# Kernel tuning notes

Measured on AMD Instinct MI355X. Metric: run time of the kernel, lower is better.

The kernel has to match this reference:

```python
import jax, jax.numpy as jnp
import numpy as np

NUM_HEADS = 16
HEAD_DIM = 64
TAU = 0.07
EPS = 1e-12  # torch F.normalize eps


def setup_inputs() -> dict:
    key = jax.random.key(0)
    ks = jax.random.split(key, 12)
    B, L, D = 4, 2048, 1024
    s = 1.0 / np.sqrt(D)
    inp = {
        'q': jax.random.normal(ks[0], (B, L, D), jnp.float32),
        'k': jax.random.normal(ks[1], (B, L, D), jnp.float32),
        'v': jax.random.normal(ks[2], (B, L, D), jnp.float32),
        'Wq': jax.random.normal(ks[3], (D, D), jnp.float32) * s,
        'bq': jax.random.normal(ks[4], (D,), jnp.float32) * 0.01,
        'Wk': jax.random.normal(ks[5], (D, D), jnp.float32) * s,
        'bk': jax.random.normal(ks[6], (D,), jnp.float32) * 0.01,
        'Wv': jax.random.normal(ks[7], (D, D), jnp.float32) * s,
        'bv': jax.random.normal(ks[8], (D,), jnp.float32) * 0.01,
        'Wo': jax.random.normal(ks[9], (D, D), jnp.float32) * s,
        'bo': jax.random.normal(ks[10], (D,), jnp.float32) * 0.01,
    }
    return inp


def _split(x):
    b, l, d = x.shape
    return x.reshape(b, l, NUM_HEADS, HEAD_DIM).transpose(0, 2, 1, 3)  # [b,h,l,dh]


def _l2norm(x):
    n = jnp.sqrt(jnp.sum(x * x, axis=-1, keepdims=True))
    return x / jnp.maximum(n, EPS)


def reference(q, k, v, Wq, bq, Wk, bk, Wv, bv, Wo, bo):
    # Linear projections (torch Linear: y = x @ W.T + b)
    qh = _l2norm(_split(q @ Wq.T + bq))
    kh = _l2norm(_split(k @ Wk.T + bk))
    vh = _split(v @ Wv.T + bv)
    scores = jnp.einsum('bhqd,bhkd->bhqk', qh, kh) / max(TAU, 1e-6)
    attn = jax.nn.softmax(scores, axis=-1)  # dropout = identity in eval
    out = jnp.einsum('bhqk,bhkd->bhqd', attn, vh)
    b, h, l, dh = out.shape
    merged = out.transpose(0, 2, 1, 3).reshape(b, l, h * dh)
    return merged @ Wo.T + bo
```

## Files before the change

kernel.cpp:

```cpp
#include <hip/hip_runtime.h>

#define BB 4
#define LL 2048
#define DD 1024
#define NH 16
#define DH 64
#define MM (BB*LL)

typedef _Float16 half8 __attribute__((ext_vector_type(8)));
typedef _Float16 half4 __attribute__((ext_vector_type(4)));
typedef _Float16 half2 __attribute__((ext_vector_type(2)));
typedef float floatx4 __attribute__((ext_vector_type(4)));

__device__ __forceinline__ void gload_lds16(const void* g, void* l) {
    __builtin_amdgcn_global_load_lds((const __attribute__((address_space(1))) void*)g,
                                     (__attribute__((address_space(3))) void*)l,
                                     16, 0, 0);
}

__device__ __forceinline__ floatx4 mfma16(half8 a, half8 b, floatx4 c) {
    return __builtin_amdgcn_mfma_f32_16x16x32_f16(a, b, c, 0, 0, 0);
}

__global__ __launch_bounds__(256) void cvt_f32_f16(const float* __restrict__ s,
                                                   _Float16* __restrict__ d, int n4) {
    int i = blockIdx.x * 256 + threadIdx.x;
    if (i < n4) {
        float4 f = ((const float4*)s)[i];
        half4 h;
        h[0] = (_Float16)f.x; h[1] = (_Float16)f.y;
        h[2] = (_Float16)f.z; h[3] = (_Float16)f.w;
        ((half4*)d)[i] = h;
    }
}

template <typename OutT>
__global__ __launch_bounds__(256) void gemm_nt(const _Float16* __restrict__ A,
                                               const _Float16* __restrict__ W,
                                               const float* __restrict__ bias,
                                               OutT* __restrict__ C) {
    const int K = 1024, N = 1024;
    __shared__ _Float16 As[128 * 32];
    __shared__ _Float16 Bs[128 * 32];

    int tid = threadIdx.x;
    int wave = tid >> 6, lane = tid & 63;
    int quad = lane >> 4, l15 = lane & 15;
    int wrow = (wave >> 1) * 64, wcol = (wave & 1) * 64;
    int m0 = blockIdx.y * 128;
    int n0 = blockIdx.x * 128;

    floatx4 acc[4][4] = {};

    int srow = tid >> 2, sseg = tid & 3;
    const _Float16* Ag0 = A + (size_t)(m0 + srow) * K + sseg * 8;
    const _Float16* Ag1 = Ag0 + (size_t)64 * K;
    const _Float16* Bg0 = W + (size_t)(n0 + srow) * K + sseg * 8;
    const _Float16* Bg1 = Bg0 + (size_t)64 * K;
    char* ldsA0 = (char*)As + tid * 16;
    char* ldsA1 = (char*)As + (256 + tid) * 16;
    char* ldsB0 = (char*)Bs + tid * 16;
    char* ldsB1 = (char*)Bs + (256 + tid) * 16;

    for (int kt = 0; kt < K; kt += 32) {
        __syncthreads();
        gload_lds16(Ag0 + kt, ldsA0);
        gload_lds16(Ag1 + kt, ldsA1);
        gload_lds16(Bg0 + kt, ldsB0);
        gload_lds16(Bg1 + kt, ldsB1);
        __syncthreads();

        half8 af[4], bf[4];
#pragma unroll
        for (int i = 0; i < 4; i++)
            af[i] = *(half8*)&As[(wrow + i * 16 + l15) * 32 + quad * 8];
#pragma unroll
        for (int j = 0; j < 4; j++)
            bf[j] = *(half8*)&Bs[(wcol + j * 16 + l15) * 32 + quad * 8];
#pragma unroll
        for (int i = 0; i < 4; i++)
#pragma unroll
            for (int j = 0; j < 4; j++)
                acc[i][j] = mfma16(af[i], bf[j], acc[i][j]);
    }

#pragma unroll
    for (int j = 0; j < 4; j++) {
        int col = n0 + wcol + j * 16 + l15;
        float bv = bias[col];
#pragma unroll
        for (int i = 0; i < 4; i++) {
#pragma unroll
            for (int r = 0; r < 4; r++) {
                int row = m0 + wrow + i * 16 + quad * 4 + r;
                float v = acc[i][j][r] + bv;
                C[(size_t)row * N + col] = (OutT)v;
            }
        }
    }
}

__global__ __launch_bounds__(256) void gemm_nt_vt(const _Float16* __restrict__ A,
                                                  const _Float16* __restrict__ W,
                                                  const float* __restrict__ bias,
                                                  _Float16* __restrict__ VtG) {
    const int K = 1024;
    __shared__ _Float16 As[128 * 32];
    __shared__ _Float16 Bs[128 * 32];

    int tid = threadIdx.x;
    int wave = tid >> 6, lane = tid & 63;
    int quad = lane >> 4, l15 = lane & 15;
    int wrow = (wave >> 1) * 64, wcol = (wave & 1) * 64;
    int m0 = blockIdx.y * 128;
    int n0 = blockIdx.x * 128;

    floatx4 acc[4][4] = {};

    int srow = tid >> 2, sseg = tid & 3;
    const _Float16* Ag0 = A + (size_t)(m0 + srow) * K + sseg * 8;
    const _Float16* Ag1 = Ag0 + (size_t)64 * K;
    const _Float16* Bg0 = W + (size_t)(n0 + srow) * K + sseg * 8;
    const _Float16* Bg1 = Bg0 + (size_t)64 * K;
    char* ldsA0 = (char*)As + tid * 16;
    char* ldsA1 = (char*)As + (256 + tid) * 16;
    char* ldsB0 = (char*)Bs + tid * 16;
    char* ldsB1 = (char*)Bs + (256 + tid) * 16;

    for (int kt = 0; kt < K; kt += 32) {
        __syncthreads();
        gload_lds16(Ag0 + kt, ldsA0);
        gload_lds16(Ag1 + kt, ldsA1);
        gload_lds16(Bg0 + kt, ldsB0);
        gload_lds16(Bg1 + kt, ldsB1);
        __syncthreads();

        half8 af[4], bf[4];
#pragma unroll
        for (int i = 0; i < 4; i++)
            af[i] = *(half8*)&As[(wrow + i * 16 + l15) * 32 + quad * 8];
#pragma unroll
        for (int j = 0; j < 4; j++)
            bf[j] = *(half8*)&Bs[(wcol + j * 16 + l15) * 32 + quad * 8];
#pragma unroll
        for (int i = 0; i < 4; i++)
#pragma unroll
            for (int j = 0; j < 4; j++)
                acc[i][j] = mfma16(af[i], bf[j], acc[i][j]);
    }

#pragma unroll
    for (int j = 0; j < 4; j++) {
        int col = n0 + wcol + j * 16 + l15;
        float bv = bias[col];
#pragma unroll
        for (int i = 0; i < 4; i++) {
#pragma unroll
            for (int r = 0; r < 4; r++) {
                int row = m0 + wrow + i * 16 + quad * 4 + r;
                int b = row >> 11, l = row & 2047;
                VtG[((size_t)((b << 10) + col)) * LL + l] = (_Float16)(acc[i][j][r] + bv);
            }
        }
    }
}

__global__ __launch_bounds__(256) void l2norm_k(_Float16* __restrict__ Qp,
                                                _Float16* __restrict__ Kp) {
    _Float16* X = blockIdx.y ? Kp : Qp;
    size_t i = ((size_t)blockIdx.x * 256 + threadIdx.x) * 8;
    half8 v = *(half8*)(X + i);
    float f[8];
    float s = 0.f;
#pragma unroll
    for (int j = 0; j < 8; j++) { f[j] = (float)v[j]; s += f[j] * f[j]; }
    s += __shfl_xor(s, 1);
    s += __shfl_xor(s, 2);
    s += __shfl_xor(s, 4);
    float sc = 1.0f / fmaxf(sqrtf(s), 1e-12f);
#pragma unroll
    for (int j = 0; j < 8; j++) v[j] = (_Float16)(f[j] * sc);
    *(half8*)(X + i) = v;
}

__global__ __launch_bounds__(256) void attn_k(const _Float16* __restrict__ Q,
                                              const _Float16* __restrict__ K,
                                              const _Float16* __restrict__ VtG,
                                              _Float16* __restrict__ Mg) {
    __shared__ _Float16 Ks[64 * 64];
    __shared__ _Float16 Vt[64 * 64];
    __shared__ _Float16 Ps[128 * 64];
    __shared__ float lsum[128];

    const float C2 = 20.60992915555662f;
    const float OFF = 6.0f;

    int tid = threadIdx.x, wave = tid >> 6, lane = tid & 63;
    int quad = lane >> 4, l15 = lane & 15;
    int bh = blockIdx.y;
    int b = bh >> 4, h = bh & 15;
    int q0 = blockIdx.x * 128;
    size_t rowBase = (size_t)b * LL;
    int colBase = h * 64;
    int wq = wave * 32;
    int sw = l15 & 7;

    half8 qf[2][2];
#pragma unroll
    for (int ib = 0; ib < 2; ib++)
#pragma unroll
        for (int ks = 0; ks < 2; ks++)
            qf[ib][ks] = *(const half8*)(Q + (rowBase + q0 + wq + ib * 16 + l15) * DD +
                                         colBase + ks * 32 + quad * 8);

    const _Float16* kg[2];
    const _Float16* vg[2];
    char* kl[2];
    char* vl[2];
#pragma unroll
    for (int p = 0; p < 2; p++) {
        int s = p * 256 + tid;
        int r = s >> 3, cs = s & 7;
        int ck = cs ^ (r & 7);
        kg[p] = K + (rowBase + r) * DD + colBase + ck * 8;
        kl[p] = (char*)Ks + s * 16;
        vg[p] = VtG + ((size_t)bh * 64 + r) * LL + ck * 8;
        vl[p] = (char*)Vt + s * 16;
    }

    floatx4 oacc[2][4] = {};
    float fsum[2] = {0.f, 0.f};

    for (int kt = 0; kt < LL; kt += 64) {
        __syncthreads();
        gload_lds16(kg[0], kl[0]); kg[0] += 64 * DD;
        gload_lds16(kg[1], kl[1]); kg[1] += 64 * DD;
        gload_lds16(vg[0], vl[0]); vg[0] += 64;
        gload_lds16(vg[1], vl[1]); vg[1] += 64;
        __syncthreads();

        floatx4 st[2][4] = {};
#pragma unroll
        for (int ks = 0; ks < 2; ks++) {
            half8 kf[4];
#pragma unroll
            for (int jb = 0; jb < 4; jb++)
                kf[jb] = *(half8*)&Ks[(jb * 16 + l15) * 64 + (((ks * 4 + quad) ^ sw) * 8)];
#pragma unroll
            for (int ib = 0; ib < 2; ib++)
#pragma unroll
                for (int jb = 0; jb < 4; jb++)
                    st[ib][jb] = mfma16(kf[jb], qf[ib][ks], st[ib][jb]);
        }

#pragma unroll
        for (int ib = 0; ib < 2; ib++) {
#pragma unroll
            for (int jb = 0; jb < 4; jb++) {
                float e0 = __builtin_amdgcn_exp2f(st[ib][jb][0] * C2 - OFF);
                float e1 = __builtin_amdgcn_exp2f(st[ib][jb][1] * C2 - OFF);
                float e2 = __builtin_amdgcn_exp2f(st[ib][jb][2] * C2 - OFF);
                float e3 = __builtin_amdgcn_exp2f(st[ib][jb][3] * C2 - OFF);
                fsum[ib] += (e0 + e1) + (e2 + e3);
                half2 p01 = __builtin_bit_cast(half2, __builtin_amdgcn_cvt_pkrtz(e0, e1));
                half2 p23 = __builtin_bit_cast(half2, __builtin_amdgcn_cvt_pkrtz(e2, e3));
                half4 pk; pk[0] = p01[0]; pk[1] = p01[1]; pk[2] = p23[0]; pk[3] = p23[1];
                int chunk = (jb * 2 + (quad >> 1)) ^ sw;
                *(half4*)((char*)Ps + (wq + ib * 16 + l15) * 128 + chunk * 16 + (quad & 1) * 8) = pk;
            }
        }

#pragma unroll
        for (int kb = 0; kb < 2; kb++) {
            half8 pf[2];
#pragma unroll
            for (int ib = 0; ib < 2; ib++)
                pf[ib] = *(half8*)&Ps[(wq + ib * 16 + l15) * 64 + (((kb * 4 + quad) ^ sw) * 8)];
#pragma unroll
            for (int jb = 0; jb < 4; jb++) {
                half8 vf = *(half8*)&Vt[(jb * 16 + l15) * 64 + (((kb * 4 + quad) ^ sw) * 8)];
#pragma unroll
                for (int ib = 0; ib < 2; ib++)
                    oacc[ib][jb] = mfma16(pf[ib], vf, oacc[ib][jb]);
            }
        }
    }

#pragma unroll
    for (int ib = 0; ib < 2; ib++) {
        float v = fsum[ib];
        v += __shfl_xor(v, 16);
        v += __shfl_xor(v, 32);
        lsum[wq + ib * 16 + l15] = v;
    }
#pragma unroll
    for (int ib = 0; ib < 2; ib++) {
#pragma unroll
        for (int r = 0; r < 4; r++) {
            float inv = 1.0f / lsum[wq + ib * 16 + quad * 4 + r];
            int qrow = q0 + wq + ib * 16 + quad * 4 + r;
#pragma unroll
            for (int jb = 0; jb < 4; jb++) {
                float v = oacc[ib][jb][r] * inv;
                Mg[(rowBase + qrow) * DD + colBase + jb * 16 + l15] = (_Float16)v;
            }
        }
    }
}

extern "C" void kernel_launch(void* const* d_in, const int* in_sizes, int n_in,
                              void* d_out, int out_size, void* d_ws, size_t ws_size,
                              hipStream_t stream) {
    (void)in_sizes; (void)n_in; (void)out_size; (void)ws_size;
    const float* q  = (const float*)d_in[0];
    const float* k  = (const float*)d_in[1];
    const float* v  = (const float*)d_in[2];
    const float* Wq = (const float*)d_in[3];
    const float* bq = (const float*)d_in[4];
    const float* Wk = (const float*)d_in[5];
    const float* bk = (const float*)d_in[6];
    const float* Wv = (const float*)d_in[7];
    const float* bv = (const float*)d_in[8];
    const float* Wo = (const float*)d_in[9];
    const float* bo = (const float*)d_in[10];

    const size_t NQKV = (size_t)MM * DD;
    const size_t NW = (size_t)DD * DD;

    _Float16* q16  = (_Float16*)d_ws;
    _Float16* k16  = q16 + NQKV;
    _Float16* v16  = k16 + NQKV;
    _Float16* wq16 = v16 + NQKV;
    _Float16* wk16 = wq16 + NW;
    _Float16* wv16 = wk16 + NW;
    _Float16* wo16 = wv16 + NW;
    _Float16* Qp   = wo16 + NW;
    _Float16* Kp   = Qp + NQKV;
    _Float16* VtG  = Kp + NQKV;
    _Float16* Mg   = VtG + NQKV;

    cvt_f32_f16<<<dim3(NQKV / 4 / 256), dim3(256), 0, stream>>>(q, q16, NQKV / 4);
    cvt_f32_f16<<<dim3(NQKV / 4 / 256), dim3(256), 0, stream>>>(k, k16, NQKV / 4);
    cvt_f32_f16<<<dim3(NQKV / 4 / 256), dim3(256), 0, stream>>>(v, v16, NQKV / 4);
    cvt_f32_f16<<<dim3(NW / 4 / 256), dim3(256), 0, stream>>>(Wq, wq16, NW / 4);
    cvt_f32_f16<<<dim3(NW / 4 / 256), dim3(256), 0, stream>>>(Wk, wk16, NW / 4);
    cvt_f32_f16<<<dim3(NW / 4 / 256), dim3(256), 0, stream>>>(Wv, wv16, NW / 4);
    cvt_f32_f16<<<dim3(NW / 4 / 256), dim3(256), 0, stream>>>(Wo, wo16, NW / 4);

    dim3 ggrid(1024 / 128, MM / 128);
    gemm_nt<_Float16><<<ggrid, dim3(256), 0, stream>>>(q16, wq16, bq, Qp);
    gemm_nt<_Float16><<<ggrid, dim3(256), 0, stream>>>(k16, wk16, bk, Kp);
    gemm_nt_vt<<<ggrid, dim3(256), 0, stream>>>(v16, wv16, bv, VtG);

    l2norm_k<<<dim3(NQKV / 8 / 256, 2), dim3(256), 0, stream>>>(Qp, Kp);

    attn_k<<<dim3(LL / 128, BB * NH), dim3(256), 0, stream>>>(Qp, Kp, VtG, Mg);

    gemm_nt<float><<<ggrid, dim3(256), 0, stream>>>(Mg, wo16, bo, (float*)d_out);
}
```

Baseline: 400.8 us.

## Merge conversions, batch QKV projections, fuse L2 norm into GEMM epilogue

Replaces the seven f32→f16 conversion launches with one kernel that dispatches by block index. The three QKV projection GEMMs become a single launch with a 24-wide grid. The per-head L2 normalization is computed in the GEMM epilogue with a 16-lane shuffle reduction over each 64-column head slice. This removes launch overheads and the separate l2norm pass that re-read and re-wrote Q and K. The cost is a larger epilogue and branch divergence by block type.

```diff
diff --git a/kernel.cpp b/kernel.cpp
--- a/kernel.cpp
+++ b/kernel.cpp
@@ -22,24 +22,52 @@
     return __builtin_amdgcn_mfma_f32_16x16x32_f16(a, b, c, 0, 0, 0);
 }
 
-__global__ __launch_bounds__(256) void cvt_f32_f16(const float* __restrict__ s,
-                                                   _Float16* __restrict__ d, int n4) {
-    int i = blockIdx.x * 256 + threadIdx.x;
-    if (i < n4) {
-        float4 f = ((const float4*)s)[i];
-        half4 h;
-        h[0] = (_Float16)f.x; h[1] = (_Float16)f.y;
-        h[2] = (_Float16)f.z; h[3] = (_Float16)f.w;
-        ((half4*)d)[i] = h;
-    }
-}
-
-template <typename OutT>
-__global__ __launch_bounds__(256) void gemm_nt(const _Float16* __restrict__ A,
-                                               const _Float16* __restrict__ W,
-                                               const float* __restrict__ bias,
-                                               OutT* __restrict__ C) {
-    const int K = 1024, N = 1024;
+__global__ __launch_bounds__(256) void cvt_all(const float* __restrict__ q,
+                                               const float* __restrict__ k,
+                                               const float* __restrict__ v,
+                                               const float* __restrict__ Wq,
+                                               const float* __restrict__ Wk,
+                                               const float* __restrict__ Wv,
+                                               const float* __restrict__ Wo,
+                                               _Float16* __restrict__ dst) {
+    const int BIG = 8192;
+    const int SML = 1024;
+    const size_t NQKV = (size_t)MM * DD;
+    const size_t NW = (size_t)DD * DD;
+    int b = blockIdx.x;
+    const float* src;
+    size_t off;
+    int lb;
+    if (b < 3 * BIG) {
+        int t = b / BIG;
+        src = t == 0 ? q : (t == 1 ? k : v);
+        off = (size_t)t * NQKV;
+        lb = b - t * BIG;
+    } else {
+        int t = (b - 3 * BIG) / SML;
+        src = t == 0 ? Wq : (t == 1 ? Wk : (t == 2 ? Wv : Wo));
+        off = 3 * NQKV + (size_t)t * NW;
+        lb = b - 3 * BIG - t * SML;
+    }
+    size_t i = (size_t)lb * 256 + threadIdx.x;
+    float4 f = ((const float4*)src)[i];
+    half4 h;
+    h[0] = (_Float16)f.x; h[1] = (_Float16)f.y;
+    h[2] = (_Float16)f.z; h[3] = (_Float16)f.w;
+    ((half4*)(dst + off))[i] = h;
+}
+
+__global__ __launch_bounds__(256) void gemm_qkv(const _Float16* __restrict__ qkv16,
+                                                const _Float16* __restrict__ wq,
+                                                const _Float16* __restrict__ wk,
+                                                const _Float16* __restrict__ wv,
+                                                const float* __restrict__ bq,
+                                                const float* __restrict__ bk,
+                                                const float* __restrict__ bv,
+                                                _Float16* __restrict__ Qp,
+                                                _Float16* __restrict__ Kp,
+                                                _Float16* __restrict__ VtG) {
+    const int K = 1024;
     __shared__ _Float16 As[128 * 32];
     __shared__ _Float16 Bs[128 * 32];
 
@@ -47,8 +75,14 @@
     int wave = tid >> 6, lane = tid & 63;
     int quad = lane >> 4, l15 = lane & 15;
     int wrow = (wave >> 1) * 64, wcol = (wave & 1) * 64;
+    int bx = blockIdx.x;
+    int which = bx >> 3;
     int m0 = blockIdx.y * 128;
-    int n0 = blockIdx.x * 128;
+    int n0 = (bx & 7) * 128;
+
+    const _Float16* A = qkv16 + (size_t)which * ((size_t)MM * DD);
+    const _Float16* W = which == 0 ? wq : (which == 1 ? wk : wv);
+    const float* bias = which == 0 ? bq : (which == 1 ? bk : bv);
 
     floatx4 acc[4][4] = {};
 
@@ -86,25 +120,57 @@
 
 #pragma unroll
     for (int j = 0; j < 4; j++) {
-        int col = n0 + wcol + j * 16 + l15;
-        float bv = bias[col];
+        float bv_ = bias[n0 + wcol + j * 16 + l15];
+#pragma unroll
+        for (int i = 0; i < 4; i++)
+#pragma unroll
+            for (int r = 0; r < 4; r++) acc[i][j][r] += bv_;
+    }
+
+    if (which < 2) {
+        _Float16* C = which == 0 ? Qp : Kp;
 #pragma unroll
         for (int i = 0; i < 4; i++) {
 #pragma unroll
             for (int r = 0; r < 4; r++) {
+                float s = 0.f;
+#pragma unroll
+                for (int j = 0; j < 4; j++) s += acc[i][j][r] * acc[i][j][r];
+                s += __shfl_xor(s, 1);
+                s += __shfl_xor(s, 2);
+                s += __shfl_xor(s, 4);
+                s += __shfl_xor(s, 8);
+                float inv = 1.0f / fmaxf(sqrtf(s), 1e-12f);
                 int row = m0 + wrow + i * 16 + quad * 4 + r;
-                float v = acc[i][j][r] + bv;
-                C[(size_t)row * N + col] = (OutT)v;
-            }
-        }
-    }
-}
-
-__global__ __launch_bounds__(256) void gemm_nt_vt(const _Float16* __restrict__ A,
-                                                  const _Float16* __restrict__ W,
-                                                  const float* __restrict__ bias,
-                                                  _Float16* __restrict__ VtG) {
-    const int K = 1024;
+#pragma unroll
+                for (int j = 0; j < 4; j++) {
+                    int col = n0 + wcol + j * 16 + l15;
+                    C[(size_t)row * DD + col] = (_Float16)(acc[i][j][r] * inv);
+                }
+            }
+        }
+    } else {
+#pragma unroll
+        for (int j = 0; j < 4; j++) {
+            int col = n0 + wcol + j * 16 + l15;
+#pragma unroll
+            for (int i = 0; i < 4; i++) {
+#pragma unroll
+                for (int r = 0; r < 4; r++) {
+                    int row = m0 + wrow + i * 16 + quad * 4 + r;
+                    int b = row >> 11, l = row & 2047;
+                    VtG[((size_t)((b << 10) + col)) * LL + l] = (_Float16)acc[i][j][r];
+                }
+            }
+        }
+    }
+}
+
+__global__ __launch_bounds__(256) void gemm_out(const _Float16* __restrict__ A,
+                                                const _Float16* __restrict__ W,
+                                                const float* __restrict__ bias,
+                                                float* __restrict__ C) {
+    const int K = 1024, N = 1024;
     __shared__ _Float16 As[128 * 32];
     __shared__ _Float16 Bs[128 * 32];
 
@@ -158,29 +224,10 @@
 #pragma unroll
             for (int r = 0; r < 4; r++) {
                 int row = m0 + wrow + i * 16 + quad * 4 + r;
-                int b = row >> 11, l = row & 2047;
-                VtG[((size_t)((b << 10) + col)) * LL + l] = (_Float16)(acc[i][j][r] + bv);
-            }
-        }
-    }
-}
-
-__global__ __launch_bounds__(256) void l2norm_k(_Float16* __restrict__ Qp,
-                                                _Float16* __restrict__ Kp) {
-    _Float16* X = blockIdx.y ? Kp : Qp;
-    size_t i = ((size_t)blockIdx.x * 256 + threadIdx.x) * 8;
-    half8 v = *(half8*)(X + i);
-    float f[8];
-    float s = 0.f;
-#pragma unroll
-    for (int j = 0; j < 8; j++) { f[j] = (float)v[j]; s += f[j] * f[j]; }
-    s += __shfl_xor(s, 1);
-    s += __shfl_xor(s, 2);
-    s += __shfl_xor(s, 4);
-    float sc = 1.0f / fmaxf(sqrtf(s), 1e-12f);
-#pragma unroll
-    for (int j = 0; j < 8; j++) v[j] = (_Float16)(f[j] * sc);
-    *(half8*)(X + i) = v;
+                C[(size_t)row * N + col] = acc[i][j][r] + bv;
+            }
+        }
+    }
 }
 
 __global__ __launch_bounds__(256) void attn_k(const _Float16* __restrict__ Q,
@@ -338,23 +385,14 @@
     _Float16* Kp   = Qp + NQKV;
     _Float16* VtG  = Kp + NQKV;
     _Float16* Mg   = VtG + NQKV;
-
-    cvt_f32_f16<<<dim3(NQKV / 4 / 256), dim3(256), 0, stream>>>(q, q16, NQKV / 4);
-    cvt_f32_f16<<<dim3(NQKV / 4 / 256), dim3(256), 0, stream>>>(k, k16, NQKV / 4);
-    cvt_f32_f16<<<dim3(NQKV / 4 / 256), dim3(256), 0, stream>>>(v, v16, NQKV / 4);
-    cvt_f32_f16<<<dim3(NW / 4 / 256), dim3(256), 0, stream>>>(Wq, wq16, NW / 4);
-    cvt_f32_f16<<<dim3(NW / 4 / 256), dim3(256), 0, stream>>>(Wk, wk16, NW / 4);
-    cvt_f32_f16<<<dim3(NW / 4 / 256), dim3(256), 0, stream>>>(Wv, wv16, NW / 4);
-    cvt_f32_f16<<<dim3(NW / 4 / 256), dim3(256), 0, stream>>>(Wo, wo16, NW / 4);
-
-    dim3 ggrid(1024 / 128, MM / 128);
-    gemm_nt<_Float16><<<ggrid, dim3(256), 0, stream>>>(q16, wq16, bq, Qp);
-    gemm_nt<_Float16><<<ggrid, dim3(256), 0, stream>>>(k16, wk16, bk, Kp);
-    gemm_nt_vt<<<ggrid, dim3(256), 0, stream>>>(v16, wv16, bv, VtG);
-
-    l2norm_k<<<dim3(NQKV / 8 / 256, 2), dim3(256), 0, stream>>>(Qp, Kp);
+    (void)k16; (void)v16;
+
+    cvt_all<<<dim3(3 * 8192 + 4 * 1024), dim3(256), 0, stream>>>(q, k, v, Wq, Wk, Wv, Wo, q16);
+
+    gemm_qkv<<<dim3(24, MM / 128), dim3(256), 0, stream>>>(q16, wq16, wk16, wv16,
+                                                           bq, bk, bv, Qp, Kp, VtG);
 
     attn_k<<<dim3(LL / 128, BB * NH), dim3(256), 0, stream>>>(Qp, Kp, VtG, Mg);
 
-    gemm_nt<float><<<ggrid, dim3(256), 0, stream>>>(Mg, wo16, bo, (float*)d_out);
-}
+    gemm_out<<<dim3(1024 / 128, MM / 128), dim3(256), 0, stream>>>(Mg, wo16, bo, (float*)d_out);
+}
```

Result: faster. 364.7 us (-9.0%).
